# Kernel optimization log

Measured on AMD Instinct MI355X. Metric: run time of the kernel, lower is better.

Reference implementation:

```python
import jax, jax.numpy as jnp
import numpy as np


def _update_cv(features, labels, CoVariance, Ave, Amount):
    """Segment-reduce form of EstimatorCV.update_CV.
    features [M,A] (detached), labels [M] int, state: CoVariance/Ave [C,A], Amount [C].
    """
    C = CoVariance.shape[0]
    M = features.shape[0]
    counts = jax.ops.segment_sum(jnp.ones((M,), features.dtype), labels, num_segments=C)  # onehot.sum(0)
    cnt_safe = jnp.where(counts == 0, 1.0, counts)[:, None]                               # Amount_CxA clamp
    sum_f = jax.ops.segment_sum(features, labels, num_segments=C)                         # [C,A]
    ave = sum_f / cnt_safe                                                                # ave_CxA
    var = jax.ops.segment_sum((features - ave[labels]) ** 2, labels, num_segments=C) / cnt_safe
    denom = counts + Amount
    w = jnp.where(denom == 0, 0.0, counts / jnp.where(denom == 0, 1.0, denom))[:, None]   # weight_CV, NaN->0
    additional = w * (1.0 - w) * (Ave - ave) ** 2
    cov_new = CoVariance * (1.0 - w) + var * w + additional
    ave_new = Ave * (1.0 - w) + ave * w
    amount_new = Amount + counts
    return cov_new, ave_new, amount_new


def _isda_aug(weight, y, labels, cv, ratio):
    """weight [C,A], y [M,C], labels [M], cv [C,A].
    sigma2[n,c] = ratio * sum_a (W[c,a]-W[lab_n,a])^2 * cv[lab_n,a], computed via fused
    einsums instead of materializing [M,C,A].
    """
    mask = labels == 255
    lab = jnp.where(mask, 0, labels)
    Wk = weight[lab]          # [M,A]
    cv_n = cv[lab]            # [M,A]
    t1 = jnp.einsum('na,ca->nc', cv_n, weight ** 2)
    t2 = jnp.einsum('na,ca->nc', cv_n * Wk, weight)
    t3 = jnp.sum(cv_n * Wk ** 2, axis=1, keepdims=True)
    sigma2 = ratio * (t1 - 2.0 * t2 + t3)
    valid = (~mask).astype(y.dtype)[:, None]
    return y + 0.5 * sigma2 * valid


def setup_inputs() -> dict:
    key = jax.random.key(0)
    k1, k2, k3, k4 = jax.random.split(key, 4)
    N, A, H, W, C = 4, 512, 128, 128, 19
    return {
        'features': jax.random.normal(k1, (N, A, H, W), dtype=jnp.float32),
        'y': jax.random.normal(k2, (N, C, H, W), dtype=jnp.float32),
        'target_x': jax.random.randint(k3, (N, 1, H, W), 0, C, dtype=jnp.int64),
        'weight': jax.random.normal(k4, (C, A), dtype=jnp.float32) * 0.05,
        'CoVariance': jnp.zeros((C, A), dtype=jnp.float32),
        'Ave': jnp.zeros((C, A), dtype=jnp.float32),
        'Amount': jnp.zeros((C,), dtype=jnp.float32),
        'ratio': jnp.float32(0.5),
    }


def reference(features, y, target_x, weight, CoVariance, Ave, Amount, ratio):
    N, A, H, W = features.shape
    C = weight.shape[0]
    # nearest interpolate to (H, W) is identity since target is already at (H, W)
    labels = target_x.reshape(N * H * W)
    f = jnp.transpose(features, (0, 2, 3, 1)).reshape(N * H * W, A)
    yf = jnp.transpose(y, (0, 2, 3, 1)).reshape(N * H * W, C)
    cov_new, _, _ = _update_cv(jax.lax.stop_gradient(f), labels, CoVariance, Ave, Amount)
    aug = _isda_aug(weight, yf, labels, jax.lax.stop_gradient(cov_new), ratio)
    return jnp.transpose(aug.reshape(N, H, W, C), (0, 3, 1, 2))
```

## Files before the change

kernel.cpp:

```cpp
#include <hip/hip_runtime.h>

#define N_DIM 4
#define A_DIM 512
#define C_DIM 19
#define HW    16384
#define A_PAD 516

__global__ __launch_bounds__(256) void reduce_kernel(const float* __restrict__ feat,
                                                     const int*   __restrict__ labels,
                                                     float* __restrict__ gsum,
                                                     float* __restrict__ gsq) {
    const int b = blockIdx.x;
    const int n = b >> 9;
    const int a = b & (A_DIM - 1);
    const float4* f4 = (const float4*)(feat + ((size_t)(n * A_DIM + a)) * HW);
    const int4*   l4 = (const int4*)(labels + n * HW);

    const int tid = threadIdx.x;

    float s[C_DIM];
    float q[C_DIM];
    #pragma unroll
    for (int c = 0; c < C_DIM; ++c) { s[c] = 0.f; q[c] = 0.f; }

    #pragma unroll 2
    for (int i = tid; i < HW / 4; i += 256) {
        float4 f = f4[i];
        int4   lb = l4[i];
        #pragma unroll
        for (int c = 0; c < C_DIM; ++c) {
            float sx = (lb.x == c) ? f.x : 0.f;
            float sy = (lb.y == c) ? f.y : 0.f;
            float sz = (lb.z == c) ? f.z : 0.f;
            float sw = (lb.w == c) ? f.w : 0.f;
            s[c] += sx + sy + sz + sw;
            q[c] = fmaf(sx, f.x, q[c]);
            q[c] = fmaf(sy, f.y, q[c]);
            q[c] = fmaf(sz, f.z, q[c]);
            q[c] = fmaf(sw, f.w, q[c]);
        }
    }

    #pragma unroll
    for (int c = 0; c < C_DIM; ++c) {
        #pragma unroll
        for (int off = 32; off >= 1; off >>= 1) {
            s[c] += __shfl_xor(s[c], off);
            q[c] += __shfl_xor(q[c], off);
        }
    }
    if ((tid & 63) == 0) {
        #pragma unroll
        for (int c = 0; c < C_DIM; ++c) {
            atomicAdd(&gsum[c * A_DIM + a], s[c]);
            atomicAdd(&gsq[c * A_DIM + a], q[c]);
        }
    }
}

__global__ __launch_bounds__(256) void count_kernel(const int* __restrict__ labels,
                                                    float* __restrict__ gcnt) {
    __shared__ float s_cnt[4][20];
    const int tid = threadIdx.x;
    const int w = tid >> 6;
    if (tid < 80) ((float*)s_cnt)[tid] = 0.f;
    __syncthreads();
    const int4* l4 = (const int4*)(labels + blockIdx.x * HW);
    for (int i = tid; i < HW / 4; i += 256) {
        int4 lb = l4[i];
        if ((unsigned)lb.x < C_DIM) atomicAdd(&s_cnt[w][lb.x], 1.f);
        if ((unsigned)lb.y < C_DIM) atomicAdd(&s_cnt[w][lb.y], 1.f);
        if ((unsigned)lb.z < C_DIM) atomicAdd(&s_cnt[w][lb.z], 1.f);
        if ((unsigned)lb.w < C_DIM) atomicAdd(&s_cnt[w][lb.w], 1.f);
    }
    __syncthreads();
    if (tid < C_DIM) {
        float cn = s_cnt[0][tid] + s_cnt[1][tid] + s_cnt[2][tid] + s_cnt[3][tid];
        atomicAdd(&gcnt[tid], cn);
    }
}

__global__ __launch_bounds__(512) void finalize_kernel(const float* __restrict__ gsum,
                                                       const float* __restrict__ gsq,
                                                       const float* __restrict__ gcnt,
                                                       const float* __restrict__ CoV,
                                                       const float* __restrict__ Ave,
                                                       const float* __restrict__ Amount,
                                                       const float* __restrict__ weight,
                                                       const float* __restrict__ ratio_p,
                                                       float* __restrict__ S) {
    alignas(16) __shared__ float s_cov[C_DIM][A_PAD];
    alignas(16) __shared__ float s_w[C_DIM][A_PAD];
    __shared__ float s_wcv[C_DIM];
    __shared__ float s_inv[C_DIM];

    const int tid = threadIdx.x;
    if (tid < C_DIM) {
        float cnt = gcnt[tid];
        float cs  = (cnt == 0.f) ? 1.f : cnt;
        float denom = cnt + Amount[tid];
        s_wcv[tid] = (denom == 0.f) ? 0.f : cnt / denom;
        s_inv[tid] = 1.f / cs;
    }
    __syncthreads();

    for (int idx = tid; idx < C_DIM * A_DIM; idx += 512) {
        const int c = idx >> 9;
        const int a = idx & (A_DIM - 1);
        float inv = s_inv[c];
        float sm  = gsum[idx];
        float ave = sm * inv;
        float var = (gsq[idx] - sm * ave) * inv;
        float wcv = s_wcv[c];
        float d   = Ave[idx] - ave;
        float cov = CoV[idx] * (1.f - wcv) + var * wcv + wcv * (1.f - wcv) * d * d;
        s_cov[c][a] = cov;
        s_w[c][a]   = weight[idx];
    }
    __syncthreads();

    const float ratio = *ratio_p;
    for (int e = tid; e < C_DIM * C_DIM; e += 512) {
        const int k = e / C_DIM;
        const int c = e % C_DIM;
        const float4* cv4 = (const float4*)&s_cov[k][0];
        const float4* wc4 = (const float4*)&s_w[c][0];
        const float4* wk4 = (const float4*)&s_w[k][0];
        float acc = 0.f;
        for (int a4 = 0; a4 < A_DIM / 4; ++a4) {
            float4 cv = cv4[a4];
            float4 wc = wc4[a4];
            float4 wk = wk4[a4];
            float dx = wc.x - wk.x, dy = wc.y - wk.y;
            float dz = wc.z - wk.z, dw = wc.w - wk.w;
            acc += cv.x * dx * dx + cv.y * dy * dy + cv.z * dz * dz + cv.w * dw * dw;
        }
        S[e] = ratio * acc;
    }
}

__global__ __launch_bounds__(256) void apply_kernel(const float* __restrict__ y,
                                                    const int*   __restrict__ labels,
                                                    const float* __restrict__ S,
                                                    float* __restrict__ out) {
    __shared__ float s_S[C_DIM * C_DIM];
    const int tid = threadIdx.x;
    for (int i = tid; i < C_DIM * C_DIM; i += 256) s_S[i] = S[i];
    __syncthreads();

    const int g = blockIdx.x * 256 + tid;
    const int per_n = C_DIM * (HW / 4);
    const int n = g / per_n;
    const int rem = g - n * per_n;
    const int c = rem >> 12;
    const int hw4 = rem & 4095;

    float4 yv = ((const float4*)y)[g];
    int4 lb = ((const int4*)(labels + n * HW))[hw4];
    float4 r;
    {
        int l = lb.x; bool v = (l != 255); l = ((unsigned)l < C_DIM) ? l : 0;
        r.x = yv.x + (v ? 0.5f * s_S[l * C_DIM + c] : 0.f);
    }
    {
        int l = lb.y; bool v = (l != 255); l = ((unsigned)l < C_DIM) ? l : 0;
        r.y = yv.y + (v ? 0.5f * s_S[l * C_DIM + c] : 0.f);
    }
    {
        int l = lb.z; bool v = (l != 255); l = ((unsigned)l < C_DIM) ? l : 0;
        r.z = yv.z + (v ? 0.5f * s_S[l * C_DIM + c] : 0.f);
    }
    {
        int l = lb.w; bool v = (l != 255); l = ((unsigned)l < C_DIM) ? l : 0;
        r.w = yv.w + (v ? 0.5f * s_S[l * C_DIM + c] : 0.f);
    }
    ((float4*)out)[g] = r;
}

extern "C" void kernel_launch(void* const* d_in, const int* in_sizes, int n_in,
                              void* d_out, int out_size, void* d_ws, size_t ws_size,
                              hipStream_t stream) {
    const float* feat   = (const float*)d_in[0];
    const float* y      = (const float*)d_in[1];
    const int*   labels = (const int*)d_in[2];
    const float* weight = (const float*)d_in[3];
    const float* CoV    = (const float*)d_in[4];
    const float* Ave    = (const float*)d_in[5];
    const float* Amount = (const float*)d_in[6];
    const float* ratio  = (const float*)d_in[7];

    float* out  = (float*)d_out;
    float* ws   = (float*)d_ws;
    float* gsum = ws;
    float* gsq  = ws + C_DIM * A_DIM;
    float* gcnt = ws + 2 * C_DIM * A_DIM;
    float* S    = gcnt + 32;

    const size_t zero_bytes = (size_t)(2 * C_DIM * A_DIM + 32 + C_DIM * C_DIM) * sizeof(float);
    hipMemsetAsync(d_ws, 0, zero_bytes, stream);

    count_kernel<<<N_DIM, 256, 0, stream>>>(labels, gcnt);
    reduce_kernel<<<N_DIM * A_DIM, 256, 0, stream>>>(feat, labels, gsum, gsq);
    finalize_kernel<<<1, 512, 0, stream>>>(gsum, gsq, gcnt, CoV, Ave, Amount, weight, ratio, S);
    apply_kernel<<<(N_DIM * C_DIM * (HW / 4)) / 256, 256, 0, stream>>>(y, labels, S, out);
}
```

Baseline: 269.6 us.

## Use per-thread LDS histograms, fold counting into reduce, fuse finalize with apply

The reduce kernel replaces its 19-way predicated register accumulation with per-thread shared-memory histograms updated by LDS atomics. It writes per-batch partial sums so no global atomics or memset are needed, and the a==0 blocks compute label counts, removing the separate count kernel. The finalize and apply kernels are merged into one 512-block kernel in which every block redundantly recomputes the 19x19 S matrix before applying it with a grid-stride loop. This cuts launches and ALU work, at the cost of redundant S computation per block and the LDS atomic throughput of the histogram path.

```diff
diff --git a/kernel.cpp b/kernel.cpp
--- a/kernel.cpp
+++ b/kernel.cpp
@@ -4,177 +4,209 @@
 #define A_DIM 512
 #define C_DIM 19
 #define HW    16384
+#define HIST_STRIDE 39
 #define A_PAD 516
+#define CA    (C_DIM * A_DIM)
 
 __global__ __launch_bounds__(256) void reduce_kernel(const float* __restrict__ feat,
                                                      const int*   __restrict__ labels,
-                                                     float* __restrict__ gsum,
-                                                     float* __restrict__ gsq) {
+                                                     float* __restrict__ gsum_part,
+                                                     float* __restrict__ gsq_part,
+                                                     float* __restrict__ gcnt_part) {
     const int b = blockIdx.x;
     const int n = b >> 9;
     const int a = b & (A_DIM - 1);
     const float4* f4 = (const float4*)(feat + ((size_t)(n * A_DIM + a)) * HW);
     const int4*   l4 = (const int4*)(labels + n * HW);
 
+    __shared__ float hist[256 * HIST_STRIDE];
+    __shared__ float s_cnt[4][20];
+
     const int tid = threadIdx.x;
-
-    float s[C_DIM];
-    float q[C_DIM];
+    float* h = hist + tid * HIST_STRIDE;
     #pragma unroll
-    for (int c = 0; c < C_DIM; ++c) { s[c] = 0.f; q[c] = 0.f; }
-
-    #pragma unroll 2
-    for (int i = tid; i < HW / 4; i += 256) {
-        float4 f = f4[i];
-        int4   lb = l4[i];
+    for (int j = 0; j < HIST_STRIDE; ++j) h[j] = 0.f;
+
+    const bool do_cnt = (a == 0);
+    float cnt[C_DIM];
+    #pragma unroll
+    for (int c = 0; c < C_DIM; ++c) cnt[c] = 0.f;
+
+    float4 f  = f4[tid];
+    int4   lb = l4[tid];
+    for (int ii = 0; ii < 16; ++ii) {
+        float4 fc = f; int4 lc = lb;
+        if (ii < 15) { f = f4[tid + (ii + 1) * 256]; lb = l4[tid + (ii + 1) * 256]; }
+        { int l = lc.x; bool v = (unsigned)l < 19u; int as = v ? l : 38, aq = v ? l + 19 : 38;
+          atomicAdd(&h[as], fc.x); atomicAdd(&h[aq], fc.x * fc.x); }
+        { int l = lc.y; bool v = (unsigned)l < 19u; int as = v ? l : 38, aq = v ? l + 19 : 38;
+          atomicAdd(&h[as], fc.y); atomicAdd(&h[aq], fc.y * fc.y); }
+        { int l = lc.z; bool v = (unsigned)l < 19u; int as = v ? l : 38, aq = v ? l + 19 : 38;
+          atomicAdd(&h[as], fc.z); atomicAdd(&h[aq], fc.z * fc.z); }
+        { int l = lc.w; bool v = (unsigned)l < 19u; int as = v ? l : 38, aq = v ? l + 19 : 38;
+          atomicAdd(&h[as], fc.w); atomicAdd(&h[aq], fc.w * fc.w); }
+        if (do_cnt) {
+            #pragma unroll
+            for (int c = 0; c < C_DIM; ++c) {
+                cnt[c] += ((lc.x == c) ? 1.f : 0.f) + ((lc.y == c) ? 1.f : 0.f)
+                        + ((lc.z == c) ? 1.f : 0.f) + ((lc.w == c) ? 1.f : 0.f);
+            }
+        }
+    }
+
+    if (do_cnt) {
         #pragma unroll
         for (int c = 0; c < C_DIM; ++c) {
-            float sx = (lb.x == c) ? f.x : 0.f;
-            float sy = (lb.y == c) ? f.y : 0.f;
-            float sz = (lb.z == c) ? f.z : 0.f;
-            float sw = (lb.w == c) ? f.w : 0.f;
-            s[c] += sx + sy + sz + sw;
-            q[c] = fmaf(sx, f.x, q[c]);
-            q[c] = fmaf(sy, f.y, q[c]);
-            q[c] = fmaf(sz, f.z, q[c]);
-            q[c] = fmaf(sw, f.w, q[c]);
-        }
-    }
-
-    #pragma unroll
-    for (int c = 0; c < C_DIM; ++c) {
-        #pragma unroll
-        for (int off = 32; off >= 1; off >>= 1) {
-            s[c] += __shfl_xor(s[c], off);
-            q[c] += __shfl_xor(q[c], off);
-        }
-    }
-    if ((tid & 63) == 0) {
-        #pragma unroll
-        for (int c = 0; c < C_DIM; ++c) {
-            atomicAdd(&gsum[c * A_DIM + a], s[c]);
-            atomicAdd(&gsq[c * A_DIM + a], q[c]);
-        }
-    }
+            float x = cnt[c];
+            #pragma unroll
+            for (int off = 32; off >= 1; off >>= 1) x += __shfl_xor(x, off);
+            if ((tid & 63) == 0) s_cnt[tid >> 6][c] = x;
+        }
+    }
+    __syncthreads();
+
+    if (tid < 38) {
+        float a0 = 0.f, a1 = 0.f, a2 = 0.f, a3 = 0.f;
+        for (int u = 0; u < 256; u += 4) {
+            a0 += hist[(u    ) * HIST_STRIDE + tid];
+            a1 += hist[(u + 1) * HIST_STRIDE + tid];
+            a2 += hist[(u + 2) * HIST_STRIDE + tid];
+            a3 += hist[(u + 3) * HIST_STRIDE + tid];
+        }
+        float acc = (a0 + a1) + (a2 + a3);
+        if (tid < C_DIM) gsum_part[(n * C_DIM + tid) * A_DIM + a] = acc;
+        else             gsq_part[(n * C_DIM + (tid - C_DIM)) * A_DIM + a] = acc;
+    }
+    if (do_cnt && tid < C_DIM)
+        gcnt_part[n * 32 + tid] = s_cnt[0][tid] + s_cnt[1][tid] + s_cnt[2][tid] + s_cnt[3][tid];
 }
 
-__global__ __launch_bounds__(256) void count_kernel(const int* __restrict__ labels,
-                                                    float* __restrict__ gcnt) {
-    __shared__ float s_cnt[4][20];
-    const int tid = threadIdx.x;
-    const int w = tid >> 6;
-    if (tid < 80) ((float*)s_cnt)[tid] = 0.f;
-    __syncthreads();
-    const int4* l4 = (const int4*)(labels + blockIdx.x * HW);
-    for (int i = tid; i < HW / 4; i += 256) {
-        int4 lb = l4[i];
-        if ((unsigned)lb.x < C_DIM) atomicAdd(&s_cnt[w][lb.x], 1.f);
-        if ((unsigned)lb.y < C_DIM) atomicAdd(&s_cnt[w][lb.y], 1.f);
-        if ((unsigned)lb.z < C_DIM) atomicAdd(&s_cnt[w][lb.z], 1.f);
-        if ((unsigned)lb.w < C_DIM) atomicAdd(&s_cnt[w][lb.w], 1.f);
-    }
-    __syncthreads();
-    if (tid < C_DIM) {
-        float cn = s_cnt[0][tid] + s_cnt[1][tid] + s_cnt[2][tid] + s_cnt[3][tid];
-        atomicAdd(&gcnt[tid], cn);
-    }
-}
-
-__global__ __launch_bounds__(512) void finalize_kernel(const float* __restrict__ gsum,
-                                                       const float* __restrict__ gsq,
-                                                       const float* __restrict__ gcnt,
-                                                       const float* __restrict__ CoV,
-                                                       const float* __restrict__ Ave,
-                                                       const float* __restrict__ Amount,
-                                                       const float* __restrict__ weight,
-                                                       const float* __restrict__ ratio_p,
-                                                       float* __restrict__ S) {
+__global__ __launch_bounds__(256) void fused_kernel(const float* __restrict__ gsum_part,
+                                                    const float* __restrict__ gsq_part,
+                                                    const float* __restrict__ gcnt_part,
+                                                    const float* __restrict__ CoV,
+                                                    const float* __restrict__ Ave,
+                                                    const float* __restrict__ Amount,
+                                                    const float* __restrict__ weight,
+                                                    const float* __restrict__ ratio_p,
+                                                    const float* __restrict__ y,
+                                                    const int*   __restrict__ labels,
+                                                    float* __restrict__ out) {
     alignas(16) __shared__ float s_cov[C_DIM][A_PAD];
     alignas(16) __shared__ float s_w[C_DIM][A_PAD];
+    __shared__ float s_S[C_DIM * 20];
     __shared__ float s_wcv[C_DIM];
     __shared__ float s_inv[C_DIM];
 
     const int tid = threadIdx.x;
     if (tid < C_DIM) {
-        float cnt = gcnt[tid];
-        float cs  = (cnt == 0.f) ? 1.f : cnt;
-        float denom = cnt + Amount[tid];
-        s_wcv[tid] = (denom == 0.f) ? 0.f : cnt / denom;
+        float cn = gcnt_part[tid] + gcnt_part[32 + tid] + gcnt_part[64 + tid] + gcnt_part[96 + tid];
+        float cs = (cn == 0.f) ? 1.f : cn;
+        float denom = cn + Amount[tid];
+        s_wcv[tid] = (denom == 0.f) ? 0.f : cn / denom;
         s_inv[tid] = 1.f / cs;
     }
     __syncthreads();
 
-    for (int idx = tid; idx < C_DIM * A_DIM; idx += 512) {
-        const int c = idx >> 9;
-        const int a = idx & (A_DIM - 1);
-        float inv = s_inv[c];
-        float sm  = gsum[idx];
-        float ave = sm * inv;
-        float var = (gsq[idx] - sm * ave) * inv;
-        float wcv = s_wcv[c];
-        float d   = Ave[idx] - ave;
-        float cov = CoV[idx] * (1.f - wcv) + var * wcv + wcv * (1.f - wcv) * d * d;
-        s_cov[c][a] = cov;
-        s_w[c][a]   = weight[idx];
-    }
-    __syncthreads();
-
-    const float ratio = *ratio_p;
-    for (int e = tid; e < C_DIM * C_DIM; e += 512) {
-        const int k = e / C_DIM;
-        const int c = e % C_DIM;
-        const float4* cv4 = (const float4*)&s_cov[k][0];
-        const float4* wc4 = (const float4*)&s_w[c][0];
-        const float4* wk4 = (const float4*)&s_w[k][0];
-        float acc = 0.f;
-        for (int a4 = 0; a4 < A_DIM / 4; ++a4) {
-            float4 cv = cv4[a4];
-            float4 wc = wc4[a4];
-            float4 wk = wk4[a4];
-            float dx = wc.x - wk.x, dy = wc.y - wk.y;
-            float dz = wc.z - wk.z, dw = wc.w - wk.w;
-            acc += cv.x * dx * dx + cv.y * dy * dy + cv.z * dz * dz + cv.w * dw * dw;
-        }
-        S[e] = ratio * acc;
-    }
-}
-
-__global__ __launch_bounds__(256) void apply_kernel(const float* __restrict__ y,
-                                                    const int*   __restrict__ labels,
-                                                    const float* __restrict__ S,
-                                                    float* __restrict__ out) {
-    __shared__ float s_S[C_DIM * C_DIM];
-    const int tid = threadIdx.x;
-    for (int i = tid; i < C_DIM * C_DIM; i += 256) s_S[i] = S[i];
-    __syncthreads();
-
-    const int g = blockIdx.x * 256 + tid;
-    const int per_n = C_DIM * (HW / 4);
-    const int n = g / per_n;
-    const int rem = g - n * per_n;
-    const int c = rem >> 12;
-    const int hw4 = rem & 4095;
-
-    float4 yv = ((const float4*)y)[g];
-    int4 lb = ((const int4*)(labels + n * HW))[hw4];
-    float4 r;
+    for (int i4 = tid; i4 < CA / 4; i4 += 256) {
+        const int c   = i4 >> 7;
+        const int aa4 = i4 & 127;
+        float4 s0 = ((const float4*)gsum_part)[i4];
+        float4 s1 = ((const float4*)gsum_part)[i4 + CA / 4];
+        float4 s2 = ((const float4*)gsum_part)[i4 + 2 * (CA / 4)];
+        float4 s3 = ((const float4*)gsum_part)[i4 + 3 * (CA / 4)];
+        float4 q0 = ((const float4*)gsq_part)[i4];
+        float4 q1 = ((const float4*)gsq_part)[i4 + CA / 4];
+        float4 q2 = ((const float4*)gsq_part)[i4 + 2 * (CA / 4)];
+        float4 q3 = ((const float4*)gsq_part)[i4 + 3 * (CA / 4)];
+        float4 cvv = ((const float4*)CoV)[i4];
+        float4 avv = ((const float4*)Ave)[i4];
+        float4 wv  = ((const float4*)weight)[i4];
+        const float inv = s_inv[c], wcv = s_wcv[c], om = 1.f - wcv;
+        float4 res;
+        {
+            float sm = s0.x + s1.x + s2.x + s3.x, sq = q0.x + q1.x + q2.x + q3.x;
+            float ave = sm * inv, var = (sq - sm * ave) * inv, d = avv.x - ave;
+            res.x = cvv.x * om + var * wcv + wcv * om * d * d;
+        }
+        {
+            float sm = s0.y + s1.y + s2.y + s3.y, sq = q0.y + q1.y + q2.y + q3.y;
+            float ave = sm * inv, var = (sq - sm * ave) * inv, d = avv.y - ave;
+            res.y = cvv.y * om + var * wcv + wcv * om * d * d;
+        }
+        {
+            float sm = s0.z + s1.z + s2.z + s3.z, sq = q0.z + q1.z + q2.z + q3.z;
+            float ave = sm * inv, var = (sq - sm * ave) * inv, d = avv.z - ave;
+            res.z = cvv.z * om + var * wcv + wcv * om * d * d;
+        }
+        {
+            float sm = s0.w + s1.w + s2.w + s3.w, sq = q0.w + q1.w + q2.w + q3.w;
+            float ave = sm * inv, var = (sq - sm * ave) * inv, d = avv.w - ave;
+            res.w = cvv.w * om + var * wcv + wcv * om * d * d;
+        }
+        *(float4*)&s_cov[c][aa4 * 4] = res;
+        *(float4*)&s_w[c][aa4 * 4]   = wv;
+    }
+    __syncthreads();
+
     {
-        int l = lb.x; bool v = (l != 255); l = ((unsigned)l < C_DIM) ? l : 0;
-        r.x = yv.x + (v ? 0.5f * s_S[l * C_DIM + c] : 0.f);
-    }
-    {
-        int l = lb.y; bool v = (l != 255); l = ((unsigned)l < C_DIM) ? l : 0;
-        r.y = yv.y + (v ? 0.5f * s_S[l * C_DIM + c] : 0.f);
-    }
-    {
-        int l = lb.z; bool v = (l != 255); l = ((unsigned)l < C_DIM) ? l : 0;
-        r.z = yv.z + (v ? 0.5f * s_S[l * C_DIM + c] : 0.f);
-    }
-    {
-        int l = lb.w; bool v = (l != 255); l = ((unsigned)l < C_DIM) ? l : 0;
-        r.w = yv.w + (v ? 0.5f * s_S[l * C_DIM + c] : 0.f);
-    }
-    ((float4*)out)[g] = r;
+        const float ratio = *ratio_p;
+        const int lane = tid & 63;
+        const int wv   = tid >> 6;
+        const int rep  = lane / C_DIM;
+        const int c    = lane % C_DIM;
+        const int kbase = wv * 5;
+        float acc[5];
+        #pragma unroll
+        for (int kk = 0; kk < 5; ++kk) acc[kk] = 0.f;
+        for (int j = 0; j < 43; ++j) {
+            const int a4 = rep + 3 * j;
+            if (rep < 3 && a4 < 128) {
+                float4 wc = *(const float4*)&s_w[c][a4 * 4];
+                #pragma unroll
+                for (int kk = 0; kk < 5; ++kk) {
+                    int k = kbase + kk; if (k > 18) k = 18;
+                    float4 cv = *(const float4*)&s_cov[k][a4 * 4];
+                    float4 wk = *(const float4*)&s_w[k][a4 * 4];
+                    float dx = wc.x - wk.x, dy = wc.y - wk.y;
+                    float dz = wc.z - wk.z, dw = wc.w - wk.w;
+                    acc[kk] = fmaf(cv.x, dx * dx, acc[kk]);
+                    acc[kk] = fmaf(cv.y, dy * dy, acc[kk]);
+                    acc[kk] = fmaf(cv.z, dz * dz, acc[kk]);
+                    acc[kk] = fmaf(cv.w, dw * dw, acc[kk]);
+                }
+            }
+        }
+        #pragma unroll
+        for (int kk = 0; kk < 5; ++kk) {
+            const int k = kbase + kk;
+            float v1 = __shfl(acc[kk], lane + 19);
+            float v2 = __shfl(acc[kk], lane + 38);
+            if (lane < C_DIM && k < C_DIM) s_S[k * 20 + lane] = ratio * (acc[kk] + v1 + v2);
+        }
+    }
+    __syncthreads();
+
+    const int total4 = N_DIM * C_DIM * (HW / 4);
+    const int per_n  = C_DIM * (HW / 4);
+    for (int g = blockIdx.x * 256 + tid; g < total4; g += (int)gridDim.x * 256) {
+        const int n   = g / per_n;
+        const int rem = g - n * per_n;
+        const int c   = rem >> 12;
+        const int hw4 = rem & 4095;
+        float4 yv = ((const float4*)y)[g];
+        int4 lbv = ((const int4*)(labels + n * HW))[hw4];
+        float4 r;
+        { int l = lbv.x; bool v = (l != 255); int lu = ((unsigned)l < 19u) ? l : 0;
+          r.x = yv.x + (v ? 0.5f * s_S[lu * 20 + c] : 0.f); }
+        { int l = lbv.y; bool v = (l != 255); int lu = ((unsigned)l < 19u) ? l : 0;
+          r.y = yv.y + (v ? 0.5f * s_S[lu * 20 + c] : 0.f); }
+        { int l = lbv.z; bool v = (l != 255); int lu = ((unsigned)l < 19u) ? l : 0;
+          r.z = yv.z + (v ? 0.5f * s_S[lu * 20 + c] : 0.f); }
+        { int l = lbv.w; bool v = (l != 255); int lu = ((unsigned)l < 19u) ? l : 0;
+          r.w = yv.w + (v ? 0.5f * s_S[lu * 20 + c] : 0.f); }
+        ((float4*)out)[g] = r;
+    }
 }
 
 extern "C" void kernel_launch(void* const* d_in, const int* in_sizes, int n_in,
@@ -189,18 +221,13 @@
     const float* Amount = (const float*)d_in[6];
     const float* ratio  = (const float*)d_in[7];
 
-    float* out  = (float*)d_out;
-    float* ws   = (float*)d_ws;
-    float* gsum = ws;
-    float* gsq  = ws + C_DIM * A_DIM;
-    float* gcnt = ws + 2 * C_DIM * A_DIM;
-    float* S    = gcnt + 32;
-
-    const size_t zero_bytes = (size_t)(2 * C_DIM * A_DIM + 32 + C_DIM * C_DIM) * sizeof(float);
-    hipMemsetAsync(d_ws, 0, zero_bytes, stream);
-
-    count_kernel<<<N_DIM, 256, 0, stream>>>(labels, gcnt);
-    reduce_kernel<<<N_DIM * A_DIM, 256, 0, stream>>>(feat, labels, gsum, gsq);
-    finalize_kernel<<<1, 512, 0, stream>>>(gsum, gsq, gcnt, CoV, Ave, Amount, weight, ratio, S);
-    apply_kernel<<<(N_DIM * C_DIM * (HW / 4)) / 256, 256, 0, stream>>>(y, labels, S, out);
+    float* out       = (float*)d_out;
+    float* ws        = (float*)d_ws;
+    float* gsum_part = ws;
+    float* gsq_part  = ws + 4 * CA;
+    float* gcnt_part = ws + 8 * CA;
+
+    reduce_kernel<<<N_DIM * A_DIM, 256, 0, stream>>>(feat, labels, gsum_part, gsq_part, gcnt_part);
+    fused_kernel<<<512, 256, 0, stream>>>(gsum_part, gsq_part, gcnt_part, CoV, Ave, Amount,
+                                          weight, ratio, y, labels, out);
 }
```

After: 557.7 us. 107% more time.
